# Kernel tuning notes

Measured on AMD Instinct MI355X. Metric: run time of the kernel, lower is better.

Reference implementation:

```python
import jax, jax.numpy as jnp
import numpy as np
from jax import lax

DIM = 1024
BATCH = 16
WIDTH = 2048
DECAY = 0.99


def setup_inputs() -> dict:
    key = jax.random.key(0)
    k1, k2, k3, k4 = jax.random.split(key, 4)
    scale = 1.0 / np.sqrt(DIM)
    x = jax.random.normal(k1, (BATCH, WIDTH, DIM), dtype=jnp.float32)
    state = jnp.zeros((BATCH, DIM), dtype=jnp.float32)
    Wv = jax.random.normal(k2, (DIM, DIM), dtype=jnp.float32) * scale
    Wr = jax.random.normal(k3, (DIM, DIM), dtype=jnp.float32) * scale
    Wc = jax.random.normal(k4, (DIM, DIM), dtype=jnp.float32) * scale
    return {"x": x, "state": state, "Wv": Wv, "Wr": Wr, "Wc": Wc}


def reference(x, state, Wv, Wr, Wc):
    # x: [B, W, D], state: [B, D]; fixed-decay RWKV recurrence along width.
    decay = jnp.asarray(DECAY, dtype=x.dtype)
    one_minus = jnp.asarray(1.0, dtype=x.dtype) - decay
    v = jnp.einsum('bwd,de->bwe', x, Wv)                 # value projection
    r = jax.nn.sigmoid(jnp.einsum('bwd,de->bwe', x, Wr))  # receptance

    # scan over width (time) axis: elems shaped [W, B, D]
    def step(s_prev, inp):
        v_t, r_t, x_t = inp
        s_curr = decay * s_prev + one_minus * v_t
        y_t = x_t + r_t * s_curr
        return s_curr, y_t

    elems = (jnp.swapaxes(v, 0, 1), jnp.swapaxes(r, 0, 1), jnp.swapaxes(x, 0, 1))
    new_state, y_t = lax.scan(step, state, elems)
    y = jnp.swapaxes(y_t, 0, 1)                          # [B, W, D]
    y = y + jnp.einsum('bwd,de->bwe', y, Wc)             # minimal channel mix
    return y, new_state
```

## Files before the change

kernel.cpp:

```cpp
#include <hip/hip_runtime.h>
#include <hip/hip_bf16.h>
#include <math.h>


#define MROWS 32768
#define NCHUNK 16
#define CHUNKL 128
#define DECAY_F 0.99f
#define OM_F 0.01f

typedef __attribute__((ext_vector_type(8))) short short8;
typedef __attribute__((ext_vector_type(4))) float floatx4;

using bf16 = __hip_bfloat16;
using bf162 = __hip_bfloat162;

__device__ __forceinline__ void async_copy16(const void* g, void* l) {
  __builtin_amdgcn_global_load_lds(
      (const __attribute__((address_space(1))) unsigned int*)g,
      (__attribute__((address_space(3))) unsigned int*)l, 16, 0, 0);
}

#define S_BARRIER() asm volatile("s_barrier" ::: "memory")
#define VMCNT6()                                                               \
  do {                                                                         \
    asm volatile("s_waitcnt vmcnt(6)" ::: "memory");                           \
    __builtin_amdgcn_sched_barrier(0);                                         \
  } while (0)
#define VMCNT0()                                                               \
  do {                                                                         \
    asm volatile("s_waitcnt vmcnt(0)" ::: "memory");                           \
    __builtin_amdgcn_sched_barrier(0);                                         \
  } while (0)
#define LGKM0()                                                                \
  do {                                                                         \
    asm volatile("s_waitcnt lgkmcnt(0)" ::: "memory");                         \
    __builtin_amdgcn_sched_barrier(0);                                         \
  } while (0)

__global__ void prep_x(const float* __restrict__ X, bf16* __restrict__ Xb) {
  const int idx = blockIdx.x * 256 + threadIdx.x;
  const float4 v = ((const float4*)X)[idx];
  union { ushort4 u; bf16 h[4]; } pk;
  pk.h[0] = __float2bfloat16(v.x);
  pk.h[1] = __float2bfloat16(v.y);
  pk.h[2] = __float2bfloat16(v.z);
  pk.h[3] = __float2bfloat16(v.w);
  ((ushort4*)Xb)[idx] = pk.u;
}

__global__ void prep_weights(const float* __restrict__ Wv,
                             const float* __restrict__ Wr,
                             const float* __restrict__ Wc,
                             bf16* __restrict__ WT) {
  __shared__ float tile[32][33];
  const int bk = blockIdx.x * 32;
  const int bn = blockIdx.y * 32;
  const float* src;
  int nbase = bn;
  if (bn < 1024)      { src = Wv; }
  else if (bn < 2048) { src = Wr; nbase = bn - 1024; }
  else                { src = Wc; nbase = bn - 2048; }
  const int tx = threadIdx.x;
  const int ty = threadIdx.y;
  #pragma unroll
  for (int i = ty; i < 32; i += 8)
    tile[i][tx] = src[(size_t)(bk + i) * 1024 + nbase + tx];
  __syncthreads();
  #pragma unroll
  for (int i = ty; i < 32; i += 8)
    WT[(size_t)(bn + i) * 1024 + bk + tx] = __float2bfloat16(tile[tx][i]);
}


#define MFMA16(MB, FA)                                                         \
  __builtin_amdgcn_s_setprio(1);                                               \
  _Pragma("unroll")                                                            \
  for (int nf = 0; nf < 4; ++nf) {                                             \
    acc[MB][nf] = __builtin_amdgcn_mfma_f32_16x16x32_bf16(                     \
        FA[0][0], fb[nf][0], acc[MB][nf], 0, 0, 0);                            \
    acc[MB + 1][nf] = __builtin_amdgcn_mfma_f32_16x16x32_bf16(                 \
        FA[1][0], fb[nf][0], acc[MB + 1][nf], 0, 0, 0);                        \
  }                                                                            \
  _Pragma("unroll")                                                            \
  for (int nf = 0; nf < 4; ++nf) {                                             \
    acc[MB][nf] = __builtin_amdgcn_mfma_f32_16x16x32_bf16(                     \
        FA[0][1], fb[nf][1], acc[MB][nf], 0, 0, 0);                            \
    acc[MB + 1][nf] = __builtin_amdgcn_mfma_f32_16x16x32_bf16(                 \
        FA[1][1], fb[nf][1], acc[MB + 1][nf], 0, 0, 0);                        \
  }                                                                            \
  __builtin_amdgcn_s_setprio(0);

#define READA(FA, MB, PTR)                                                     \
  FA[0][0] = *(const short8*)((PTR) + (MB) * 2048 + lk0);                      \
  FA[0][1] = *(const short8*)((PTR) + (MB) * 2048 + lk1);                      \
  FA[1][0] = *(const short8*)((PTR) + ((MB) + 1) * 2048 + lk0);                \
  FA[1][1] = *(const short8*)((PTR) + ((MB) + 1) * 2048 + lk1);

#define READB(PTR)                                                             \
  _Pragma("unroll")                                                            \
  for (int nf = 0; nf < 4; ++nf) {                                             \
    fb[nf][0] = *(const short8*)((PTR) + nf * 2048 + lk0);                     \
    fb[nf][1] = *(const short8*)((PTR) + nf * 2048 + lk1);                     \
  }

#define STAGE(GP, LOFF)                                                        \
  do {                                                                         \
    async_copy16((GP), lds + (LOFF) + wb);                                     \
    async_copy16((GP) + (size_t)64 * 2048, lds + (LOFF) + 8192 + wb);          \
  } while (0)

template <int MODE>
__global__ __launch_bounds__(512, 2) void gemm8(const bf16* __restrict__ Ab,
                                                const bf16* __restrict__ Bw,
                                                bf16* __restrict__ Vout,
                                                bf16* __restrict__ Rout,
                                                float* __restrict__ Fout) {
  extern __shared__ char lds[];
  constexpr int NTN = (MODE == 0) ? 8 : 4;

  const int nwg = gridDim.x;
  const int id = blockIdx.x;
  const int wg = (id & 7) * (nwg >> 3) + (id >> 3);
  const int mt = wg / NTN, nt = wg % NTN;
  const int m0 = mt * 256, n0 = nt * 256;

  const int t = threadIdx.x;
  const int l = t & 63, w = t >> 6;
  const int wm = w >> 2, wn = w & 3;
  const int wb = w * 1024;

  const int sgrow = w * 8 + (l >> 3);
  const int sgcol = ((l & 7) ^ ((l >> 3) & 7)) * 16;
  const char* gA0 = (const char*)Ab + (size_t)(m0 + sgrow) * 2048 + sgcol;
  const char* gA1 = gA0 + (size_t)128 * 2048;
  const char* gB0 = (const char*)Bw + (size_t)(n0 + sgrow) * 2048 + sgcol;
  const char* gB1 = gB0 + (size_t)128 * 2048;

  const int ll = l & 15, qd = l >> 4;
  const int arow = ll * 128;
  const int lk0 = ((qd ^ (ll & 7)) << 4);
  const int lk1 = (((4 | qd) ^ (ll & 7)) << 4);
  const char* pAP = lds + wm * 16384 + arow;
  const char* pBP = lds + 32768 + (wn >> 1) * 16384 + (wn & 1) * 8192 + arow;
  const char* pAQ = pAP + 65536;
  const char* pBQ = pBP + 65536;

  floatx4 acc[8][4];
  #pragma unroll
  for (int i = 0; i < 8; ++i)
    #pragma unroll
    for (int j = 0; j < 4; ++j) acc[i][j] = (floatx4){0.f, 0.f, 0.f, 0.f};

  short8 fa01[2][2], fa23[2][2], fa45[2][2], fa67[2][2], fb[4][2];

  STAGE(gB0, 32768);         gB0 += 128;
  STAGE(gB1, 49152);         gB1 += 128;
  STAGE(gA0, 0);             gA0 += 128;
  STAGE(gA1, 16384);         gA1 += 128;
  STAGE(gB0, 65536 + 32768); gB0 += 128;
  STAGE(gB1, 65536 + 49152); gB1 += 128;
  STAGE(gA0, 65536);         gA0 += 128;
  VMCNT6();
  S_BARRIER();

  for (int j = 0; j < 8; ++j) {
    const bool full = (j < 7);
    READB(pBP);
    READA(fa01, 0, pAP);
    STAGE(gA1, 65536 + 16384); gA1 += 128;
    S_BARRIER(); LGKM0();
    MFMA16(0, fa01);
    S_BARRIER();
    READA(fa23, 2, pAP);
    READA(fa45, 4, pAP);
    if (full) { STAGE(gB0, 32768); gB0 += 128; }
    S_BARRIER(); LGKM0();
    MFMA16(2, fa23);
    S_BARRIER();
    READA(fa67, 6, pAP);
    if (full) { STAGE(gB1, 49152); gB1 += 128; }
    S_BARRIER(); LGKM0();
    MFMA16(4, fa45);
    S_BARRIER();
    if (full) { STAGE(gA0, 0); gA0 += 128; }
    MFMA16(6, fa67);
    if (full) { VMCNT6(); } else { VMCNT0(); }
    S_BARRIER();
    READB(pBQ);
    READA(fa01, 0, pAQ);
    if (full) { STAGE(gA1, 16384); gA1 += 128; }
    S_BARRIER(); LGKM0();
    MFMA16(0, fa01);
    S_BARRIER();
    READA(fa23, 2, pAQ);
    READA(fa45, 4, pAQ);
    if (full) { STAGE(gB0, 65536 + 32768); gB0 += 128; }
    S_BARRIER(); LGKM0();
    MFMA16(2, fa23);
    S_BARRIER();
    READA(fa67, 6, pAQ);
    if (full) { STAGE(gB1, 65536 + 49152); gB1 += 128; }
    S_BARRIER(); LGKM0();
    MFMA16(4, fa45);
    S_BARRIER();
    if (full) { STAGE(gA0, 65536); gA0 += 128; }
    MFMA16(6, fa67);
    if (full) { VMCNT6(); S_BARRIER(); }
  }

  const int orow0 = m0 + wm * 128 + (l >> 4) * 4;
  const int ocol = n0 + wn * 64 + ll;
  if constexpr (MODE == 0) {
    const bool isr = (n0 >= 1024);
    bf16* outp = isr ? Rout : Vout;
    const int oc = isr ? (ocol - 1024) : ocol;
    #pragma unroll
    for (int mf = 0; mf < 8; ++mf) {
      #pragma unroll
      for (int i = 0; i < 4; ++i) {
        const size_t ro = (size_t)(orow0 + mf * 16 + i) * 1024 + oc;
        #pragma unroll
        for (int nf = 0; nf < 4; ++nf) {
          float cv = acc[mf][nf][i];
          if (isr) cv = 1.0f / (1.0f + __expf(-cv));
          outp[ro + nf * 16] = __float2bfloat16(cv);
        }
      }
    }
  } else {
    #pragma unroll
    for (int mf = 0; mf < 8; ++mf) {
      #pragma unroll
      for (int i = 0; i < 4; ++i) {
        const size_t ro = (size_t)(orow0 + mf * 16 + i) * 1024 + ocol;
        #pragma unroll
        for (int nf = 0; nf < 4; ++nf) {
          const size_t o = ro + nf * 16;
          Fout[o] = __bfloat162float(Ab[o]) + acc[mf][nf][i];
        }
      }
    }
  }
}

__global__ void scan_partial(const bf16* __restrict__ V, float* __restrict__ sl) {
  const int idx = blockIdx.x * 256 + threadIdx.x;
  const int d2 = idx & 511;
  const int c = (idx >> 9) & 15;
  const int b = idx >> 13;
  const bf162* V2 = (const bf162*)V;
  const size_t base = (size_t)(b * 2048 + c * 128) * 512 + d2;
  float s0 = 0.f, s1 = 0.f;
  for (int w = 0; w < CHUNKL; ++w) {
    const bf162 v = V2[base + (size_t)w * 512];
    s0 = DECAY_F * s0 + OM_F * __bfloat162float(v.x);
    s1 = DECAY_F * s1 + OM_F * __bfloat162float(v.y);
  }
  const int o = (b * 16 + c) * 1024 + d2 * 2;
  sl[o] = s0;
  sl[o + 1] = s1;
}

__global__ void scan_chunk(const float* __restrict__ state,
                           const float* __restrict__ sl,
                           float* __restrict__ sin_,
                           float* __restrict__ state_out,
                           float decayL) {
  const int idx = blockIdx.x * 256 + threadIdx.x;
  const int d = idx & 1023;
  const int b = idx >> 10;
  float s = state[idx];
  #pragma unroll
  for (int c = 0; c < NCHUNK; ++c) {
    const int o = (b * 16 + c) * 1024 + d;
    sin_[o] = s;
    s = decayL * s + sl[o];
  }
  state_out[idx] = s;
}

__global__ void scan_apply(const bf16* __restrict__ Xb,
                           const bf16* __restrict__ R,
                           const float* __restrict__ sin_,
                           bf16* __restrict__ VY) {
  const int idx = blockIdx.x * 256 + threadIdx.x;
  const int d2 = idx & 511;
  const int c = (idx >> 9) & 15;
  const int b = idx >> 13;
  const bf162* R2 = (const bf162*)R;
  const bf162* X2 = (const bf162*)Xb;
  bf162* VY2 = (bf162*)VY;
  const size_t base = (size_t)(b * 2048 + c * 128) * 512 + d2;
  const int so = (b * 16 + c) * 1024 + d2 * 2;
  float s0 = sin_[so], s1 = sin_[so + 1];
  for (int w = 0; w < CHUNKL; ++w) {
    const size_t off = base + (size_t)w * 512;
    const bf162 v = VY2[off];
    const bf162 r = R2[off];
    const bf162 xx = X2[off];
    s0 = DECAY_F * s0 + OM_F * __bfloat162float(v.x);
    s1 = DECAY_F * s1 + OM_F * __bfloat162float(v.y);
    const float y0 = __bfloat162float(xx.x) + __bfloat162float(r.x) * s0;
    const float y1 = __bfloat162float(xx.y) + __bfloat162float(r.y) * s1;
    bf162 o;
    o.x = __float2bfloat16(y0);
    o.y = __float2bfloat16(y1);
    VY2[off] = o;
  }
}

extern "C" void kernel_launch(void* const* d_in, const int* in_sizes, int n_in,
                              void* d_out, int out_size, void* d_ws, size_t ws_size,
                              hipStream_t stream) {
  const float* x     = (const float*)d_in[0];
  const float* state = (const float*)d_in[1];
  const float* Wv    = (const float*)d_in[2];
  const float* Wr    = (const float*)d_in[3];
  const float* Wc    = (const float*)d_in[4];

  float* y_out = (float*)d_out;
  float* state_out = y_out + (size_t)MROWS * 1024;

  char* ws = (char*)d_ws;
  bf16* WT   = (bf16*)ws;
  bf16* Xb   = (bf16*)(ws + ((size_t)6 << 20));
  bf16* Vbuf = (bf16*)(ws + ((size_t)70 << 20));
  bf16* Rbuf = (bf16*)(ws + ((size_t)134 << 20));
  float* sl  = (float*)(ws + ((size_t)198 << 20));
  float* sin_ = (float*)(ws + ((size_t)199 << 20));
  bf16* WcT = WT + (size_t)2048 * 1024;

  const float decayL = (float)pow(0.99, (double)CHUNKL);

  static bool g_cfg = false;
  if (!g_cfg) {
    auto kf0 = gemm8<0>;
    auto kf1 = gemm8<1>;
    (void)hipFuncSetAttribute((const void*)kf0,
                              hipFuncAttributeMaxDynamicSharedMemorySize, 131072);
    (void)hipFuncSetAttribute((const void*)kf1,
                              hipFuncAttributeMaxDynamicSharedMemorySize, 131072);
    g_cfg = true;
  }

  prep_x<<<32768, 256, 0, stream>>>(x, Xb);
  prep_weights<<<dim3(32, 96), dim3(32, 8), 0, stream>>>(Wv, Wr, Wc, WT);
  gemm8<0><<<1024, 512, 131072, stream>>>(Xb, WT, Vbuf, Rbuf, nullptr);
  scan_partial<<<512, 256, 0, stream>>>(Vbuf, sl);
  scan_chunk<<<64, 256, 0, stream>>>(state, sl, sin_, state_out, decayL);
  scan_apply<<<512, 256, 0, stream>>>(Xb, Rbuf, sin_, Vbuf);
  gemm8<1><<<512, 512, 131072, stream>>>(Vbuf, WcT, nullptr, nullptr, y_out);
}
```

Before: 512.3 us.

## Restructure GEMM main loop into quadrant MFMA schedule with register double-buffered fragments

```diff
diff --git a/kernel.cpp b/kernel.cpp
--- a/kernel.cpp
+++ b/kernel.cpp
@@ -22,19 +22,10 @@
 }
 
 #define S_BARRIER() asm volatile("s_barrier" ::: "memory")
-#define VMCNT6()                                                               \
+#define SCHED0() __builtin_amdgcn_sched_barrier(0)
+#define VMCNT(N)                                                               \
   do {                                                                         \
-    asm volatile("s_waitcnt vmcnt(6)" ::: "memory");                           \
-    __builtin_amdgcn_sched_barrier(0);                                         \
-  } while (0)
-#define VMCNT0()                                                               \
-  do {                                                                         \
-    asm volatile("s_waitcnt vmcnt(0)" ::: "memory");                           \
-    __builtin_amdgcn_sched_barrier(0);                                         \
-  } while (0)
-#define LGKM0()                                                                \
-  do {                                                                         \
-    asm volatile("s_waitcnt lgkmcnt(0)" ::: "memory");                         \
+    asm volatile("s_waitcnt vmcnt(" #N ")" ::: "memory");                      \
     __builtin_amdgcn_sched_barrier(0);                                         \
   } while (0)
 
@@ -73,36 +64,38 @@
 }
 
 
-#define MFMA16(MB, FA)                                                         \
+#define QMFMA(FA, FB, MB, NB)                                                  \
   __builtin_amdgcn_s_setprio(1);                                               \
   _Pragma("unroll")                                                            \
-  for (int nf = 0; nf < 4; ++nf) {                                             \
-    acc[MB][nf] = __builtin_amdgcn_mfma_f32_16x16x32_bf16(                     \
-        FA[0][0], fb[nf][0], acc[MB][nf], 0, 0, 0);                            \
-    acc[MB + 1][nf] = __builtin_amdgcn_mfma_f32_16x16x32_bf16(                 \
-        FA[1][0], fb[nf][0], acc[MB + 1][nf], 0, 0, 0);                        \
-  }                                                                            \
+  for (int mfi = 0; mfi < 4; ++mfi)                                            \
+    _Pragma("unroll")                                                          \
+    for (int nfi = 0; nfi < 2; ++nfi)                                          \
+      acc[(MB) + mfi][(NB) + nfi] = __builtin_amdgcn_mfma_f32_16x16x32_bf16(   \
+          FA[mfi][0], FB[nfi][0], acc[(MB) + mfi][(NB) + nfi], 0, 0, 0);       \
   _Pragma("unroll")                                                            \
-  for (int nf = 0; nf < 4; ++nf) {                                             \
-    acc[MB][nf] = __builtin_amdgcn_mfma_f32_16x16x32_bf16(                     \
-        FA[0][1], fb[nf][1], acc[MB][nf], 0, 0, 0);                            \
-    acc[MB + 1][nf] = __builtin_amdgcn_mfma_f32_16x16x32_bf16(                 \
-        FA[1][1], fb[nf][1], acc[MB + 1][nf], 0, 0, 0);                        \
-  }                                                                            \
+  for (int mfi = 0; mfi < 4; ++mfi)                                            \
+    _Pragma("unroll")                                                          \
+    for (int nfi = 0; nfi < 2; ++nfi)                                          \
+      acc[(MB) + mfi][(NB) + nfi] = __builtin_amdgcn_mfma_f32_16x16x32_bf16(   \
+          FA[mfi][1], FB[nfi][1], acc[(MB) + mfi][(NB) + nfi], 0, 0, 0);       \
   __builtin_amdgcn_s_setprio(0);
 
-#define READA(FA, MB, PTR)                                                     \
-  FA[0][0] = *(const short8*)((PTR) + (MB) * 2048 + lk0);                      \
-  FA[0][1] = *(const short8*)((PTR) + (MB) * 2048 + lk1);                      \
-  FA[1][0] = *(const short8*)((PTR) + ((MB) + 1) * 2048 + lk0);                \
-  FA[1][1] = *(const short8*)((PTR) + ((MB) + 1) * 2048 + lk1);
-
-#define READB(PTR)                                                             \
+#define RD_FA4(DST, PTR)                                                       \
   _Pragma("unroll")                                                            \
-  for (int nf = 0; nf < 4; ++nf) {                                             \
-    fb[nf][0] = *(const short8*)((PTR) + nf * 2048 + lk0);                     \
-    fb[nf][1] = *(const short8*)((PTR) + nf * 2048 + lk1);                     \
-  }
+  for (int f = 0; f < 4; ++f) {                                                \
+    DST[f][0] = *(const short8*)((PTR) + f * 2048 + lk0);                      \
+    DST[f][1] = *(const short8*)((PTR) + f * 2048 + lk1);                      \
+  }
+#define RD_FA2(DST, D0, MFB, PTR)                                              \
+  DST[D0][0] = *(const short8*)((PTR) + (MFB) * 2048 + lk0);                   \
+  DST[D0][1] = *(const short8*)((PTR) + (MFB) * 2048 + lk1);                   \
+  DST[(D0) + 1][0] = *(const short8*)((PTR) + ((MFB) + 1) * 2048 + lk0);       \
+  DST[(D0) + 1][1] = *(const short8*)((PTR) + ((MFB) + 1) * 2048 + lk1);
+#define RD_FB2(DST, NOFF, PTR)                                                 \
+  DST[0][0] = *(const short8*)((PTR) + (NOFF) + lk0);                          \
+  DST[0][1] = *(const short8*)((PTR) + (NOFF) + lk1);                          \
+  DST[1][0] = *(const short8*)((PTR) + (NOFF) + 2048 + lk0);                   \
+  DST[1][1] = *(const short8*)((PTR) + (NOFF) + 2048 + lk1);
 
 #define STAGE(GP, LOFF)                                                        \
   do {                                                                         \
@@ -152,61 +145,65 @@
     #pragma unroll
     for (int j = 0; j < 4; ++j) acc[i][j] = (floatx4){0.f, 0.f, 0.f, 0.f};
 
-  short8 fa01[2][2], fa23[2][2], fa45[2][2], fa67[2][2], fb[4][2];
-
-  STAGE(gB0, 32768);         gB0 += 128;
-  STAGE(gB1, 49152);         gB1 += 128;
-  STAGE(gA0, 0);             gA0 += 128;
-  STAGE(gA1, 16384);         gA1 += 128;
-  STAGE(gB0, 65536 + 32768); gB0 += 128;
-  STAGE(gB1, 65536 + 49152); gB1 += 128;
-  STAGE(gA0, 65536);         gA0 += 128;
-  VMCNT6();
+  short8 faL[4][2], faH[4][2], fbA[2][2], fbB[2][2];
+
+  STAGE(gB0, 32768);         STAGE(gB1, 49152);
+  STAGE(gA0, 0);             STAGE(gA1, 16384);
+  gB0 += 128; gB1 += 128; gA0 += 128; gA1 += 128;
+  STAGE(gB0, 65536 + 32768); STAGE(gB1, 65536 + 49152);
+  STAGE(gA0, 65536 + 0);     STAGE(gA1, 65536 + 16384);
+  gB0 += 128; gB1 += 128; gA0 += 128; gA1 += 128;
+  VMCNT(8);
   S_BARRIER();
+  RD_FA4(faL, pAP);
+  RD_FB2(fbA, 0, pBP);
 
   for (int j = 0; j < 8; ++j) {
     const bool full = (j < 7);
-    READB(pBP);
-    READA(fa01, 0, pAP);
-    STAGE(gA1, 65536 + 16384); gA1 += 128;
-    S_BARRIER(); LGKM0();
-    MFMA16(0, fa01);
-    S_BARRIER();
-    READA(fa23, 2, pAP);
-    READA(fa45, 4, pAP);
-    if (full) { STAGE(gB0, 32768); gB0 += 128; }
-    S_BARRIER(); LGKM0();
-    MFMA16(2, fa23);
-    S_BARRIER();
-    READA(fa67, 6, pAP);
-    if (full) { STAGE(gB1, 49152); gB1 += 128; }
-    S_BARRIER(); LGKM0();
-    MFMA16(4, fa45);
-    S_BARRIER();
-    if (full) { STAGE(gA0, 0); gA0 += 128; }
-    MFMA16(6, fa67);
-    if (full) { VMCNT6(); } else { VMCNT0(); }
-    S_BARRIER();
-    READB(pBQ);
-    READA(fa01, 0, pAQ);
-    if (full) { STAGE(gA1, 16384); gA1 += 128; }
-    S_BARRIER(); LGKM0();
-    MFMA16(0, fa01);
-    S_BARRIER();
-    READA(fa23, 2, pAQ);
-    READA(fa45, 4, pAQ);
-    if (full) { STAGE(gB0, 65536 + 32768); gB0 += 128; }
-    S_BARRIER(); LGKM0();
-    MFMA16(2, fa23);
-    S_BARRIER();
-    READA(fa67, 6, pAQ);
-    if (full) { STAGE(gB1, 65536 + 49152); gB1 += 128; }
-    S_BARRIER(); LGKM0();
-    MFMA16(4, fa45);
-    S_BARRIER();
-    if (full) { STAGE(gA0, 65536); gA0 += 128; }
-    MFMA16(6, fa67);
-    if (full) { VMCNT6(); S_BARRIER(); }
+    RD_FB2(fbB, 4096, pBP);
+    RD_FA2(faH, 0, 4, pAP);
+    S_BARRIER(); SCHED0();
+    QMFMA(faL, fbA, 0, 0);
+    S_BARRIER();
+    RD_FA2(faH, 2, 6, pAP);
+    S_BARRIER(); SCHED0();
+    QMFMA(faL, fbB, 0, 2);
+    S_BARRIER();
+    if (full) { STAGE(gB0, 32768); STAGE(gB1, 49152); gB0 += 128; gB1 += 128; }
+    S_BARRIER(); SCHED0();
+    QMFMA(faH, fbB, 4, 2);
+    if (full) { VMCNT(4); } else { VMCNT(0); }
+    S_BARRIER();
+    RD_FA4(faL, pAQ);
+    RD_FB2(fbB, 0, pBQ);
+    if (full) { STAGE(gA0, 0); STAGE(gA1, 16384); gA0 += 128; gA1 += 128; }
+    S_BARRIER(); SCHED0();
+    QMFMA(faH, fbA, 4, 0);
+    S_BARRIER();
+    RD_FB2(fbA, 4096, pBQ);
+    RD_FA2(faH, 0, 4, pAQ);
+    S_BARRIER(); SCHED0();
+    QMFMA(faL, fbB, 0, 0);
+    S_BARRIER();
+    RD_FA2(faH, 2, 6, pAQ);
+    S_BARRIER(); SCHED0();
+    QMFMA(faL, fbA, 0, 2);
+    S_BARRIER();
+    if (full) { STAGE(gB0, 65536 + 32768); STAGE(gB1, 65536 + 49152);
+                gB0 += 128; gB1 += 128; }
+    S_BARRIER(); SCHED0();
+    QMFMA(faH, fbA, 4, 2);
+    if (full) { VMCNT(4); }
+    S_BARRIER();
+    if (full) {
+      RD_FA4(faL, pAP);
+      RD_FB2(fbA, 0, pBP);
+      STAGE(gA0, 65536 + 0); STAGE(gA1, 65536 + 16384);
+      gA0 += 128; gA1 += 128;
+    }
+    S_BARRIER(); SCHED0();
+    QMFMA(faH, fbB, 4, 0);
+    S_BARRIER();
   }
 
   const int orow0 = m0 + wm * 128 + (l >> 4) * 4;
```

Measured after the change: 925.4 us. 80.6% more time.
